# Optimization experiments

Hardware: AMD Instinct MI355X
Metric: run time of the kernel (lower is better)

## Reference

```python
import jax, jax.numpy as jnp
import numpy as np

N = 100000
NEG_SLOPE = 0.2


def gat_layer(x, src, dst, W, a_src, a_dst, b):
    # x: [N, Fin]; src/dst: [Etot] (self-loops included); W: [Fin, Fout]
    h = x @ W                                  # [N, Fout]
    s_src = h @ a_src                          # [N] per-node source score
    s_dst = h @ a_dst                          # [N] per-node dest score
    e = jax.nn.leaky_relu(s_src[src] + s_dst[dst], NEG_SLOPE)  # [Etot]
    # segment softmax over destination neighborhoods (numerically stable)
    e_max = jax.ops.segment_max(e, dst, num_segments=N)
    ex = jnp.exp(e - e_max[dst])
    denom = jax.ops.segment_sum(ex, dst, num_segments=N)
    alpha = ex / denom[dst]                    # [Etot]
    out = jax.ops.segment_sum(alpha[:, None] * h[src], dst, num_segments=N) + b
    return out, alpha


def setup_inputs() -> dict:
    key = jax.random.key(0)
    ks = jax.random.split(key, 10)
    Fin, Fh, Fo = 128, 64, 32
    x = jax.random.normal(ks[0], (N, Fin), dtype=jnp.float32)
    edge_index = jax.random.randint(ks[1], (2, 3200000), 0, N, dtype=jnp.int32)
    # Glorot-ish scaled params
    W1 = jax.random.normal(ks[2], (Fin, Fh), dtype=jnp.float32) * (1.0 / np.sqrt(Fin))
    a_src1 = jax.random.normal(ks[3], (Fh,), dtype=jnp.float32) * (1.0 / np.sqrt(Fh))
    a_dst1 = jax.random.normal(ks[4], (Fh,), dtype=jnp.float32) * (1.0 / np.sqrt(Fh))
    b1 = jnp.zeros((Fh,), dtype=jnp.float32)
    W2 = jax.random.normal(ks[5], (Fh, Fo), dtype=jnp.float32) * (1.0 / np.sqrt(Fh))
    a_src2 = jax.random.normal(ks[6], (Fo,), dtype=jnp.float32) * (1.0 / np.sqrt(Fo))
    a_dst2 = jax.random.normal(ks[7], (Fo,), dtype=jnp.float32) * (1.0 / np.sqrt(Fo))
    b2 = jnp.zeros((Fo,), dtype=jnp.float32)
    return {"x": x, "edge_index": edge_index, "W1": W1, "a_src1": a_src1,
            "a_dst1": a_dst1, "b1": b1, "W2": W2, "a_src2": a_src2,
            "a_dst2": a_dst2, "b2": b2}


def reference(x, edge_index, W1, a_src1, a_dst1, b1, W2, a_src2, a_dst2, b2):
    # PyG GATConv default add_self_loops=True: append (i, i) for every node
    loops = jnp.arange(N, dtype=edge_index.dtype)
    src = jnp.concatenate([edge_index[0], loops])
    dst = jnp.concatenate([edge_index[1], loops])
    h1, alpha1 = gat_layer(x, src, dst, W1, a_src1, a_dst1, b1)
    h1 = jax.nn.elu(h1)
    h2, alpha2 = gat_layer(h1, src, dst, W2, a_src2, a_dst2, b2)
    return h2, alpha1, alpha2
```

## Files before the change

kernel.cpp:

```cpp
#include <hip/hip_runtime.h>
#include <hip/hip_fp16.h>
#include <float.h>

#define K1E 6528

__device__ __forceinline__ float wredmax(float v){
#pragma unroll
  for (int m = 32; m >= 1; m >>= 1) v = fmaxf(v, __shfl_xor(v, m, 64));
  return v;
}
__device__ __forceinline__ float wredsum(float v){
#pragma unroll
  for (int m = 32; m >= 1; m >>= 1) v += __shfl_xor(v, m, 64);
  return v;
}
__device__ __forceinline__ int wredsumi(int v){
#pragma unroll
  for (int m = 32; m >= 1; m >>= 1) v += __shfl_xor(v, m, 64);
  return v;
}
__device__ __forceinline__ unsigned pk2(float a, float b){
  __half2 t = __floats2half2_rn(a, b);
  return __builtin_bit_cast(unsigned, t);
}
__device__ __forceinline__ float2 upk2(unsigned u){
  return __half22float2(__builtin_bit_cast(__half2, u));
}

__global__ __launch_bounds__(256) void k_split(
    const int* __restrict__ ei, int E0, int total, int NB, int C1,
    unsigned* __restrict__ temp, int* __restrict__ tcounts, int* __restrict__ trunstart)
{
  __shared__ int cnt[512];
  __shared__ int pref[512];
  __shared__ unsigned stage[K1E];
  const int tid = threadIdx.x, blk = blockIdx.x;
  const int lo = blk * K1E, hi = min(lo + K1E, total);

  for (int i = tid; i < 512; i += 256) cnt[i] = 0;
  __syncthreads();
  for (int i = lo + tid; i < hi; i += 256){
    int d = (i < E0) ? ei[E0 + i] : (i - E0);
    atomicAdd(&cnt[d >> 8], 1);
  }
  __syncthreads();
  for (int i = tid; i < 512; i += 256) pref[i] = cnt[i];
  __syncthreads();
  for (int off = 1; off < 512; off <<= 1){
    int a0 = (tid >= off) ? pref[tid - off] : 0;
    int a1 = pref[tid + 256 - off];
    __syncthreads();
    pref[tid] += a0;
    pref[tid + 256] += a1;
    __syncthreads();
  }
  for (int i = tid; i < NB; i += 256){
    int c = cnt[i];
    int ex = pref[i] - c;
    tcounts[(size_t)i * C1 + blk] = c;
    trunstart[(size_t)i * C1 + blk] = ex;
    cnt[i] = ex;
  }
  __syncthreads();
  for (int i = lo + tid; i < hi; i += 256){
    int s, d;
    if (i < E0){ s = ei[i]; d = ei[E0 + i]; } else { s = i - E0; d = s; }
    int p = atomicAdd(&cnt[d >> 8], 1);
    stage[p] = ((unsigned)(d & 255) << 17) | (unsigned)s;
  }
  __syncthreads();
  for (int i = tid; i < hi - lo; i += 256) temp[(size_t)lo + i] = stage[i];
}

__global__ __launch_bounds__(256) void k_rowsum(
    const int* __restrict__ tcounts, int C1, int* __restrict__ totals)
{
  const int b = blockIdx.x;
  const int* row = tcounts + (size_t)b * C1;
  int s = 0;
  for (int k = threadIdx.x; k < C1; k += 256) s += row[k];
  s = wredsumi(s);
  __shared__ int ws[4];
  if ((threadIdx.x & 63) == 0) ws[threadIdx.x >> 6] = s;
  __syncthreads();
  if (threadIdx.x == 0) totals[b] = ws[0] + ws[1] + ws[2] + ws[3];
}

__global__ __launch_bounds__(512) void k_bases2(
    const int* __restrict__ totals, int NB, int total,
    int* __restrict__ bases, int* __restrict__ offs, int N)
{
  __shared__ int sc[512];
  const int t = threadIdx.x;
  int v = (t < NB) ? totals[t] : 0;
  sc[t] = v; __syncthreads();
  for (int off = 1; off < 512; off <<= 1){
    int a = (t >= off) ? sc[t - off] : 0;
    __syncthreads();
    sc[t] += a;
    __syncthreads();
  }
  if (t < NB) bases[t] = sc[t] - v;
  if (t == 0) offs[N] = total;
}

__global__ __launch_bounds__(512) void k_bucket(
    const unsigned* __restrict__ temp, const int* __restrict__ tcounts,
    const int* __restrict__ trunstart, const int* __restrict__ bases,
    int C1, int N, int* __restrict__ ssrc, int* __restrict__ offs)
{
  __shared__ int rloc[1024], rlen[1024];
  __shared__ int cnt[256], sc[256];
  const int b = blockIdx.x, t = threadIdx.x;
  const int bb = bases[b];
  const int node0 = b << 8;
  const int nnode = min(256, N - node0);

  for (int k = t; k < C1; k += 512){
    rlen[k] = tcounts[(size_t)b * C1 + k];
    rloc[k] = k * K1E + trunstart[(size_t)b * C1 + k];
  }
  if (t < 256) cnt[t] = 0;
  __syncthreads();
  for (int r = t; r < C1; r += 512){
    const int L = rlen[r], base = rloc[r];
    for (int q = 0; q < L; ++q) atomicAdd(&cnt[temp[base + q] >> 17], 1);
  }
  __syncthreads();
  if (t < 256) sc[t] = cnt[t];
  __syncthreads();
  for (int off = 1; off < 256; off <<= 1){
    int a = (t < 256 && t >= off) ? sc[t - off] : 0;
    __syncthreads();
    if (t < 256) sc[t] += a;
    __syncthreads();
  }
  if (t < 256){
    int ex = sc[t] - cnt[t];
    if (t < nnode) offs[node0 + t] = bb + ex;
    cnt[t] = ex;
  }
  __syncthreads();
  for (int r = t; r < C1; r += 512){
    const int L = rlen[r], base = rloc[r];
    for (int q = 0; q < L; ++q){
      unsigned v = temp[base + q];
      int p = atomicAdd(&cnt[v >> 17], 1);
      ssrc[bb + p] = (int)(v & 0x1FFFFu);
    }
  }
}

template<int FIN, int FOUT>
__global__ __launch_bounds__(256) void k_linear(
    const float* __restrict__ x, const float* __restrict__ W,
    const float* __restrict__ a_s, const float* __restrict__ a_d,
    __half* __restrict__ h16, float* __restrict__ s_src, float* __restrict__ s_dst, int n)
{
  constexpr int CK = 32;
  constexpr int NCH = FIN / CK;
  __shared__ float xs[CK][257];
  const int tid = threadIdx.x;
  const int node0 = blockIdx.x * 256;
  const int node = node0 + tid;
  const int nrow = min(256, n - node0);

  float acc[FOUT];
#pragma unroll
  for (int o = 0; o < FOUT; ++o) acc[o] = 0.f;

  for (int kc = 0; kc < NCH; ++kc){
    __syncthreads();
    const int r0 = tid >> 3;
    const int c4 = tid & 7;
#pragma unroll
    for (int p = 0; p < 8; ++p){
      int row = p * 32 + r0;
      if (row < nrow){
        const float4 v = *reinterpret_cast<const float4*>(
            x + (size_t)(node0 + row) * FIN + kc * CK + c4 * 4);
        xs[c4 * 4 + 0][row] = v.x;
        xs[c4 * 4 + 1][row] = v.y;
        xs[c4 * 4 + 2][row] = v.z;
        xs[c4 * 4 + 3][row] = v.w;
      }
    }
    __syncthreads();
#pragma unroll 8
    for (int k = 0; k < CK; ++k){
      float xv = xs[k][tid];
      const int kg = kc * CK + k;
#pragma unroll
      for (int o4 = 0; o4 < FOUT / 4; ++o4){
        const float4 w = *reinterpret_cast<const float4*>(W + (size_t)kg * FOUT + o4 * 4);
        acc[o4 * 4 + 0] = fmaf(xv, w.x, acc[o4 * 4 + 0]);
        acc[o4 * 4 + 1] = fmaf(xv, w.y, acc[o4 * 4 + 1]);
        acc[o4 * 4 + 2] = fmaf(xv, w.z, acc[o4 * 4 + 2]);
        acc[o4 * 4 + 3] = fmaf(xv, w.w, acc[o4 * 4 + 3]);
      }
    }
  }

  if (node < n){
    float vs = 0.f, vd = 0.f;
#pragma unroll
    for (int o4 = 0; o4 < FOUT / 4; ++o4){
      const float4 as = *reinterpret_cast<const float4*>(a_s + o4 * 4);
      const float4 ad = *reinterpret_cast<const float4*>(a_d + o4 * 4);
      vs += acc[o4*4+0]*as.x + acc[o4*4+1]*as.y + acc[o4*4+2]*as.z + acc[o4*4+3]*as.w;
      vd += acc[o4*4+0]*ad.x + acc[o4*4+1]*ad.y + acc[o4*4+2]*ad.z + acc[o4*4+3]*ad.w;
    }
#pragma unroll
    for (int c = 0; c < FOUT / 8; ++c){
      uint4 u;
      u.x = pk2(acc[c*8+0], acc[c*8+1]);
      u.y = pk2(acc[c*8+2], acc[c*8+3]);
      u.z = pk2(acc[c*8+4], acc[c*8+5]);
      u.w = pk2(acc[c*8+6], acc[c*8+7]);
      *reinterpret_cast<uint4*>(h16 + (size_t)node * FOUT + c * 8) = u;
    }
    s_src[node] = vs;
    s_dst[node] = vd;
  }
}

template<int F, bool ELU>
__global__ __launch_bounds__(256) void k_segment(
    const int* __restrict__ offs, const int* __restrict__ ssrc,
    const float* __restrict__ s_src, const float* __restrict__ s_dst,
    const __half* __restrict__ h16, const float* __restrict__ bias,
    float* __restrict__ out, float* __restrict__ gmv, float* __restrict__ invv, int n)
{
  int wid = (blockIdx.x * blockDim.x + threadIdx.x) >> 6;
  if (wid >= n) return;
  int lane = threadIdx.x & 63;
  int beg = offs[wid], end = offs[wid + 1];
  float sd = s_dst[wid];

  float m = -FLT_MAX, ss = 0.f;
  for (int j = beg + lane; j < end; j += 64){
    int s = ssrc[j];
    float e = s_src[s] + sd;
    e = (e > 0.f) ? e : 0.2f * e;
    if (e > m){ ss = ss * __expf(m - e) + 1.f; m = e; }
    else ss += __expf(e - m);
  }
  float gm = wredmax(m);
  float denom = wredsum(ss * __expf(m - gm));
  float inv = 1.f / denom;
  if (lane == 0){ gmv[wid] = gm; invv[wid] = inv; }

  constexpr int FG = F / 8;
  constexpr int ES = 64 / FG;
  int es = lane / FG, fg = lane % FG;
  float a0=0.f,a1=0.f,a2=0.f,a3=0.f,a4=0.f,a5=0.f,a6=0.f,a7=0.f;
  for (int j = beg; j < end; j += ES){
    int jj = j + es;
    if (jj < end){
      int s = ssrc[jj];
      float e = s_src[s] + sd;
      e = (e > 0.f) ? e : 0.2f * e;
      float w = __expf(e - gm) * inv;
      const uint4 hv = *reinterpret_cast<const uint4*>(h16 + (size_t)s * F + fg * 8);
      float2 f0 = upk2(hv.x), f1 = upk2(hv.y), f2 = upk2(hv.z), f3 = upk2(hv.w);
      a0 = fmaf(w, f0.x, a0); a1 = fmaf(w, f0.y, a1);
      a2 = fmaf(w, f1.x, a2); a3 = fmaf(w, f1.y, a3);
      a4 = fmaf(w, f2.x, a4); a5 = fmaf(w, f2.y, a5);
      a6 = fmaf(w, f3.x, a6); a7 = fmaf(w, f3.y, a7);
    }
  }
#pragma unroll
  for (int mm = FG; mm < 64; mm <<= 1){
    a0 += __shfl_xor(a0, mm, 64); a1 += __shfl_xor(a1, mm, 64);
    a2 += __shfl_xor(a2, mm, 64); a3 += __shfl_xor(a3, mm, 64);
    a4 += __shfl_xor(a4, mm, 64); a5 += __shfl_xor(a5, mm, 64);
    a6 += __shfl_xor(a6, mm, 64); a7 += __shfl_xor(a7, mm, 64);
  }
  if (lane < FG){
    float o[8] = {a0,a1,a2,a3,a4,a5,a6,a7};
#pragma unroll
    for (int q = 0; q < 8; ++q){
      float v = o[q] + bias[fg * 8 + q];
      if (ELU) v = (v > 0.f) ? v : (__expf(v) - 1.f);
      o[q] = v;
    }
    float4 w0 = {o[0],o[1],o[2],o[3]}, w1 = {o[4],o[5],o[6],o[7]};
    *reinterpret_cast<float4*>(out + (size_t)wid * F + fg * 8)     = w0;
    *reinterpret_cast<float4*>(out + (size_t)wid * F + fg * 8 + 4) = w1;
  }
}

__global__ __launch_bounds__(256) void k_pack(
    const float* __restrict__ ss1, const float* __restrict__ sd1,
    const float* __restrict__ gm1, const float* __restrict__ inv1,
    const float* __restrict__ ss2, const float* __restrict__ sd2,
    const float* __restrict__ gm2, const float* __restrict__ inv2,
    float2* __restrict__ ssp, float4* __restrict__ pkd, int N)
{
  int i = blockIdx.x * blockDim.x + threadIdx.x;
  if (i >= N) return;
  ssp[i] = make_float2(ss1[i], ss2[i]);
  pkd[2 * i]     = make_float4(sd1[i], gm1[i], inv1[i], sd2[i]);
  pkd[2 * i + 1] = make_float4(gm2[i], inv2[i], 0.f, 0.f);
}

__global__ __launch_bounds__(256) void k_alpha(
    const int* __restrict__ ei, int E0, int total, int G,
    const float2* __restrict__ ssp, const float4* __restrict__ pkd,
    float* __restrict__ a1, float* __restrict__ a2)
{
  const int t = blockIdx.x * blockDim.x + threadIdx.x;
  int sv[4], dv[4];
  bool ok[4];
#pragma unroll
  for (int q = 0; q < 4; ++q){
    int i = t + q * G;
    ok[q] = i < total;
    if (ok[q]){
      if (i < E0){ sv[q] = ei[i]; dv[q] = ei[E0 + i]; }
      else { sv[q] = i - E0; dv[q] = sv[q]; }
    }
  }
  float2 ssv[4]; float4 da[4], db[4];
#pragma unroll
  for (int q = 0; q < 4; ++q){
    if (ok[q]){
      ssv[q] = ssp[sv[q]];
      da[q]  = pkd[2 * dv[q]];
      db[q]  = pkd[2 * dv[q] + 1];
    }
  }
#pragma unroll
  for (int q = 0; q < 4; ++q){
    if (ok[q]){
      int i = t + q * G;
      float e1 = ssv[q].x + da[q].x;
      e1 = (e1 > 0.f) ? e1 : 0.2f * e1;
      a1[i] = __expf(e1 - da[q].y) * da[q].z;
      float e2 = ssv[q].y + da[q].w;
      e2 = (e2 > 0.f) ? e2 : 0.2f * e2;
      a2[i] = __expf(e2 - db[q].x) * db[q].y;
    }
  }
}

extern "C" void kernel_launch(void* const* d_in, const int* in_sizes, int n_in,
                              void* d_out, int out_size, void* d_ws, size_t ws_size,
                              hipStream_t stream)
{
  const float* x    = (const float*)d_in[0];
  const int*   ei   = (const int*)  d_in[1];
  const float* W1   = (const float*)d_in[2];
  const float* a_s1 = (const float*)d_in[3];
  const float* a_d1 = (const float*)d_in[4];
  const float* b1   = (const float*)d_in[5];
  const float* W2   = (const float*)d_in[6];
  const float* a_s2 = (const float*)d_in[7];
  const float* a_d2 = (const float*)d_in[8];
  const float* b2   = (const float*)d_in[9];

  const int N    = in_sizes[0] / 128;
  const int E0   = in_sizes[1] / 2;
  const int Etot = E0 + N;
  const int NB   = (N + 255) >> 8;
  const int C1   = (Etot + K1E - 1) / K1E;

  float* out_h2 = (float*)d_out;
  float* out_a1 = out_h2 + (size_t)N * 32;
  float* out_a2 = out_a1 + Etot;

  char* wsp = (char*)d_ws; size_t woff = 0;
  auto alloc = [&](size_t bytes)->void*{
    void* p = wsp + woff; woff += (bytes + 255) & ~(size_t)255; return p;
  };
  unsigned* temp     = (unsigned*)alloc((size_t)C1 * K1E * 4);
  int*      tcounts  = (int*)  alloc((size_t)NB * C1 * 4);
  int*      trunstart= (int*)  alloc((size_t)NB * C1 * 4);
  int*      totals   = (int*)  alloc((size_t)(NB + 1) * 4);
  int*      bases    = (int*)  alloc((size_t)(NB + 1) * 4);
  int*      offs     = (int*)  alloc(((size_t)N + 1) * 4);
  int*      ssrc     = (int*)  alloc((size_t)Etot * 4);
  __half*   h1       = (__half*)alloc((size_t)N * 64 * 2);
  float*    g1       = (float*)alloc((size_t)N * 64 * 4);
  __half*   h2l      = (__half*)alloc((size_t)N * 32 * 2);
  float*    s1s      = (float*)alloc((size_t)N * 4);
  float*    s1d      = (float*)alloc((size_t)N * 4);
  float*    s2s      = (float*)alloc((size_t)N * 4);
  float*    s2d      = (float*)alloc((size_t)N * 4);
  float*    gm1      = (float*)alloc((size_t)N * 4);
  float*    inv1     = (float*)alloc((size_t)N * 4);
  float*    gm2      = (float*)alloc((size_t)N * 4);
  float*    inv2     = (float*)alloc((size_t)N * 4);
  float2*   ssp      = (float2*)alloc((size_t)N * 8);
  float4*   pkd      = (float4*)alloc((size_t)N * 32);

  const int tb = 256;
  k_split<<<C1, 256, 0, stream>>>(ei, E0, Etot, NB, C1, temp, tcounts, trunstart);
  k_rowsum<<<NB, 256, 0, stream>>>(tcounts, C1, totals);
  k_bases2<<<1, 512, 0, stream>>>(totals, NB, Etot, bases, offs, N);
  k_bucket<<<NB, 512, 0, stream>>>(temp, tcounts, trunstart, bases, C1, N, ssrc, offs);

  const int nlb = (N + 255) / 256;
  k_linear<128, 64><<<nlb, 256, 0, stream>>>(x, W1, a_s1, a_d1, h1, s1s, s1d, N);
  k_segment<64, true><<<(N + 3) / 4, 256, 0, stream>>>(offs, ssrc, s1s, s1d, h1, b1, g1, gm1, inv1, N);
  k_linear<64, 32><<<nlb, 256, 0, stream>>>(g1, W2, a_s2, a_d2, h2l, s2s, s2d, N);
  k_segment<32, false><<<(N + 3) / 4, 256, 0, stream>>>(offs, ssrc, s2s, s2d, h2l, b2, out_h2, gm2, inv2, N);

  k_pack<<<nlb, 256, 0, stream>>>(s1s, s1d, gm1, inv1, s2s, s2d, gm2, inv2, ssp, pkd, N);
  const int G = (Etot + 3) / 4;
  k_alpha<<<(G + tb - 1) / tb, tb, 0, stream>>>(ei, E0, Etot, G, ssp, pkd, out_a1, out_a2);
}
```

Before: 367.4 us.

## Cache edge scores in LDS and accumulate aggregation in packed half2

The segment kernel now stores each edge's leaky-relu score in shared memory during the softmax pass, for nodes with degree up to 128. The aggregation pass reads the score back instead of gathering s_src again. Aggregation also switches from fp32 FMAs on unpacked values to packed half2 FMAs on the fp16 features, which saves conversion instructions. The cost is fp16 accumulation precision, which may cause error on high-degree nodes, plus some added LDS use and a waitcnt.

```diff
diff --git a/kernel.cpp b/kernel.cpp
--- a/kernel.cpp
+++ b/kernel.cpp
@@ -22,9 +22,6 @@
 __device__ __forceinline__ unsigned pk2(float a, float b){
   __half2 t = __floats2half2_rn(a, b);
   return __builtin_bit_cast(unsigned, t);
-}
-__device__ __forceinline__ float2 upk2(unsigned u){
-  return __half22float2(__builtin_bit_cast(__half2, u));
 }
 
 __global__ __launch_bounds__(256) void k_split(
@@ -231,44 +228,57 @@
     const __half* __restrict__ h16, const float* __restrict__ bias,
     float* __restrict__ out, float* __restrict__ gmv, float* __restrict__ invv, int n)
 {
-  int wid = (blockIdx.x * blockDim.x + threadIdx.x) >> 6;
-  if (wid >= n) return;
-  int lane = threadIdx.x & 63;
-  int beg = offs[wid], end = offs[wid + 1];
-  float sd = s_dst[wid];
-
-  float m = -FLT_MAX, ss = 0.f;
+  constexpr int CAP = 128;
+  __shared__ float ew[4][CAP];
+  const int wv = threadIdx.x >> 6;
+  const int lane = threadIdx.x & 63;
+  const int wid = (blockIdx.x * blockDim.x + threadIdx.x) >> 6;
+  const bool act = wid < n;
+  int beg = 0, end = 0;
+  float sd = 0.f;
+  if (act){ beg = offs[wid]; end = offs[wid + 1]; sd = s_dst[wid]; }
+  const int deg = end - beg;
+  const bool fit = deg <= CAP;
+
+  float m = -FLT_MAX, ssum = 0.f;
   for (int j = beg + lane; j < end; j += 64){
     int s = ssrc[j];
     float e = s_src[s] + sd;
     e = (e > 0.f) ? e : 0.2f * e;
-    if (e > m){ ss = ss * __expf(m - e) + 1.f; m = e; }
-    else ss += __expf(e - m);
-  }
+    if (fit) ew[wv][j - beg] = e;
+    if (e > m){ ssum = ssum * __expf(m - e) + 1.f; m = e; }
+    else ssum += __expf(e - m);
+  }
+  asm volatile("s_waitcnt lgkmcnt(0)" ::: "memory");
   float gm = wredmax(m);
-  float denom = wredsum(ss * __expf(m - gm));
+  float denom = wredsum(ssum * __expf(m - gm));
   float inv = 1.f / denom;
-  if (lane == 0){ gmv[wid] = gm; invv[wid] = inv; }
+  if (act && lane == 0){ gmv[wid] = gm; invv[wid] = inv; }
 
   constexpr int FG = F / 8;
   constexpr int ES = 64 / FG;
-  int es = lane / FG, fg = lane % FG;
-  float a0=0.f,a1=0.f,a2=0.f,a3=0.f,a4=0.f,a5=0.f,a6=0.f,a7=0.f;
+  const int es = lane / FG, fg = lane % FG;
+  __half2 hc0 = __float2half2_rn(0.f), hc1 = hc0, hc2 = hc0, hc3 = hc0;
   for (int j = beg; j < end; j += ES){
     int jj = j + es;
     if (jj < end){
       int s = ssrc[jj];
-      float e = s_src[s] + sd;
-      e = (e > 0.f) ? e : 0.2f * e;
+      float e;
+      if (fit) e = ew[wv][jj - beg];
+      else { e = s_src[s] + sd; e = (e > 0.f) ? e : 0.2f * e; }
       float w = __expf(e - gm) * inv;
+      __half2 w2 = __float2half2_rn(w);
       const uint4 hv = *reinterpret_cast<const uint4*>(h16 + (size_t)s * F + fg * 8);
-      float2 f0 = upk2(hv.x), f1 = upk2(hv.y), f2 = upk2(hv.z), f3 = upk2(hv.w);
-      a0 = fmaf(w, f0.x, a0); a1 = fmaf(w, f0.y, a1);
-      a2 = fmaf(w, f1.x, a2); a3 = fmaf(w, f1.y, a3);
-      a4 = fmaf(w, f2.x, a4); a5 = fmaf(w, f2.y, a5);
-      a6 = fmaf(w, f3.x, a6); a7 = fmaf(w, f3.y, a7);
-    }
-  }
+      hc0 = __hfma2(w2, __builtin_bit_cast(__half2, hv.x), hc0);
+      hc1 = __hfma2(w2, __builtin_bit_cast(__half2, hv.y), hc1);
+      hc2 = __hfma2(w2, __builtin_bit_cast(__half2, hv.z), hc2);
+      hc3 = __hfma2(w2, __builtin_bit_cast(__half2, hv.w), hc3);
+    }
+  }
+  float2 p0 = __half22float2(hc0), p1 = __half22float2(hc1),
+         p2 = __half22float2(hc2), p3 = __half22float2(hc3);
+  float a0 = p0.x, a1 = p0.y, a2 = p1.x, a3 = p1.y,
+        a4 = p2.x, a5 = p2.y, a6 = p3.x, a7 = p3.y;
 #pragma unroll
   for (int mm = FG; mm < 64; mm <<= 1){
     a0 += __shfl_xor(a0, mm, 64); a1 += __shfl_xor(a1, mm, 64);
@@ -276,7 +286,7 @@
     a4 += __shfl_xor(a4, mm, 64); a5 += __shfl_xor(a5, mm, 64);
     a6 += __shfl_xor(a6, mm, 64); a7 += __shfl_xor(a7, mm, 64);
   }
-  if (lane < FG){
+  if (act && lane < FG){
     float o[8] = {a0,a1,a2,a3,a4,a5,a6,a7};
 #pragma unroll
     for (int q = 0; q < 8; ++q){
```

After: 360.5 us. No clear change (-1.9%).
